# Performance work log

Hardware: AMD Instinct MI355X
Metric: run time of the kernel (lower is better)

The kernel has to match this reference:

```python
import jax, jax.numpy as jnp
import numpy as np

RADIUS = 5            # min(max(5, ceil(80/20)), 80) = 5
SPATIAL_SIGMA = 4.0
INTENSITY_SIGMA = 1.0
EPS_MEAN = 1e-5
EPS_DEN = 1e-6


def gaussian_kernel(radius, sigma, dtype):
    # norm.pdf(d/sigma)/norm.pdf(0) == exp(-d^2 / (2*sigma^2))
    x2 = jnp.arange(-radius, radius + 1, dtype=dtype) ** 2
    d2 = x2[:, None, None] + x2[None, :, None] + x2[None, None, :]
    k = jnp.exp(-d2 / (2.0 * sigma * sigma))
    return k[None, None]  # OIDHW: [1,1,2r+1,2r+1,2r+1]


def conv3d_same(x, kernel):
    # x: [B,1,H,W,D]; 'same' padding with radius on all spatial dims
    pad = [(RADIUS, RADIUS)] * 3
    return jax.lax.conv_general_dilated(
        x, kernel, window_strides=(1, 1, 1), padding=pad,
        dimension_numbers=('NCDHW', 'OIDHW', 'NCDHW'))


def setup_inputs() -> dict:
    key = jax.random.key(0)
    k1, k2 = jax.random.split(key)
    labels = jax.random.uniform(k1, (2, 4, 80, 80, 80), dtype=jnp.float32)
    inputs = jax.random.uniform(k2, (2, 1, 80, 80, 80), dtype=jnp.float32)
    return {"labels": labels, "inputs": inputs}


def reference(labels, inputs):
    N, K, H, W, D = labels.shape
    kernel = gaussian_kernel(RADIUS, SPATIAL_SIGMA, labels.dtype)

    probs = labels[:, :, None]          # [N,K,1,H,W,D]
    img = inputs[:, None]               # [N,1,C,H,W,D]

    # per-class mean intensity: [N,K,C,1,1,1]
    class_mean = (jnp.mean(img * probs, axis=(3, 4, 5), keepdims=True)
                  / (jnp.mean(probs, axis=(3, 4, 5), keepdims=True) + EPS_MEAN))
    diff = jnp.sum((img - class_mean) ** 2, axis=2)        # [N,K,H,W,D]
    weights = jnp.exp(-(diff ** 2) / (INTENSITY_SIGMA ** 2))  # [N,K,H,W,D]

    # batch the K independent single-channel 3D convs as [N*K,1,H,W,D]
    pw = (labels * weights).reshape(N * K, 1, H, W, D)
    w = weights.reshape(N * K, 1, H, W, D)
    conv_pw = conv3d_same(pw, kernel).reshape(N, K, H, W, D)
    conv_w = conv3d_same(w, kernel).reshape(N, K, H, W, D)

    numerator = jnp.sum(labels * conv_pw, axis=(2, 3, 4))   # [N,K]
    denominator = jnp.sum(labels * conv_w, axis=(2, 3, 4))  # [N,K]
    ratio = numerator / (denominator + EPS_DEN)

    # torch L1Loss(num/den, 0) = mean over batch N, summed over classes k
    loss = jnp.sum(jnp.mean(jnp.abs(ratio), axis=0))
    return K - loss
```

## Files before the change

### kernel.cpp

```cpp
#include <hip/hip_runtime.h>
#include <math.h>

#define RAD 5
#define SIDE 80
#define SLAB 6400
#define VOL 512000
#define NCH 8
#define NCLS 4
#define Q 20
#define TW 40
#define NT 2
#define C1 (SIDE*NT)
#define NBLK1 (NCH*C1)
#define TBS 22
#define NBLK2 1000
#define CPB 125

__constant__ float GW[11] = {
    0.45783336177161427f, 0.6065306597126334f, 0.7548396019890073f,
    0.8824969025845955f,  0.969233234476344f,  1.0f,
    0.969233234476344f,   0.8824969025845955f, 0.7548396019890073f,
    0.6065306597126334f,  0.45783336177161427f};

__device__ unsigned short g_bufT[(size_t)NCH * VOL];
__device__ float2 g_part1[NBLK1];
__device__ float2 g_part2[NBLK2];

__device__ __forceinline__ unsigned short f2bf(float f) {
    unsigned u = __float_as_uint(f);
    u += 0x7FFFu + ((u >> 16) & 1u);
    return (unsigned short)(u >> 16);
}
__device__ __forceinline__ float bf2f(unsigned short h) {
    return __uint_as_float((unsigned)h << 16);
}

__global__ void __launch_bounds__(256) convdw_sums_kernel(
        const float* __restrict__ labels, const float* __restrict__ img) {
    const int tile = blockIdx.x;
    const int c   = tile / C1;
    const int rem = tile % C1;
    const int h   = rem / NT;
    const int w0  = (rem % NT) * TW;
    const int n   = c >> 2;

    __shared__ float4 tB[(TW + 10) * TBS];
    __shared__ float sm[8];

    const float4* labc4 = (const float4*)(labels + ((size_t)c * SIDE + h) * SLAB);
    const float4* imgc4 = (const float4*)(img + ((size_t)n * SIDE + h) * SLAB);

    float sip = 0.f, sp = 0.f;
    for (int i = threadIdx.x; i < (TW + 10) * Q; i += 256) {
        const int r = i / Q, q = i - (i / Q) * Q;
        const int w = w0 - RAD + r;
        float a[20];
        #pragma unroll
        for (int j = 0; j < 20; ++j) a[j] = 0.f;
        if ((unsigned)w < SIDE) {
            const float4* row = labc4 + (size_t)w * Q;
            #pragma unroll
            for (int j = 0; j < 5; ++j) {
                int qq = q - 2 + j;
                if (qq >= 0 && qq < Q) {
                    float4 v = row[qq];
                    a[4 * j] = v.x; a[4 * j + 1] = v.y;
                    a[4 * j + 2] = v.z; a[4 * j + 3] = v.w;
                }
            }
            if (r >= RAD && r < RAD + TW) {
                float4 v = imgc4[(size_t)w * Q + q];
                sip += a[8] * v.x + a[9] * v.y + a[10] * v.z + a[11] * v.w;
                sp  += a[8] + a[9] + a[10] + a[11];
            }
        }
        float s0 = 0.f, s1 = 0.f, s2 = 0.f, s3 = 0.f;
        #pragma unroll
        for (int t = 0; t < 11; ++t) {
            float g = GW[t];
            s0 += g * a[t + 3]; s1 += g * a[t + 4];
            s2 += g * a[t + 5]; s3 += g * a[t + 6];
        }
        tB[r * TBS + q] = make_float4(s0, s1, s2, s3);
    }
    #pragma unroll
    for (int off = 32; off > 0; off >>= 1) {
        sip += __shfl_down(sip, off);
        sp  += __shfl_down(sp, off);
    }
    const int lane = threadIdx.x & 63;
    const int wid  = threadIdx.x >> 6;
    if (lane == 0) { sm[wid * 2] = sip; sm[wid * 2 + 1] = sp; }
    __syncthreads();
    if (threadIdx.x == 0)
        g_part1[tile] = make_float2(sm[0] + sm[2] + sm[4] + sm[6],
                                    sm[1] + sm[3] + sm[5] + sm[7]);
    ushort4* out4 = (ushort4*)g_bufT + ((size_t)c * VOL + (size_t)h * SIDE) / 4;
    for (int i = threadIdx.x; i < TW * Q; i += 256) {
        const int rl = i / Q, q = i - (i / Q) * Q;
        float sx = 0.f, sy = 0.f, sz = 0.f, sw = 0.f;
        #pragma unroll
        for (int t = 0; t < 11; ++t) {
            float g = GW[t];
            float4 v = tB[(rl + t) * TBS + q];
            sx += g * v.x; sy += g * v.y; sz += g * v.z; sw += g * v.w;
        }
        ushort4 o;
        o.x = f2bf(sx); o.y = f2bf(sy); o.z = f2bf(sz); o.w = f2bf(sw);
        out4[(size_t)(w0 + rl) * (SLAB / 4) + q] = o;
    }
}

__global__ void __launch_bounds__(256) convh_dot_kernel(
        const float* __restrict__ labels, const float* __restrict__ img) {
    const int c   = blockIdx.x / CPB;
    const int rem = (blockIdx.x % CPB) * 256 + threadIdx.x;
    const int hq  = rem / 1600;
    const int r2  = rem % 1600;
    const int w   = r2 / Q;
    const int q   = r2 % Q;
    const int h0  = hq * 4;
    const int n   = c >> 2;

    __shared__ float sm[8];
    __shared__ float s_mean;

    float a = 0.f, b = 0.f;
    for (int t = threadIdx.x; t < C1; t += 256) {
        float2 p = g_part1[c * C1 + t];
        a += p.x; b += p.y;
    }
    #pragma unroll
    for (int off = 32; off > 0; off >>= 1) {
        a += __shfl_down(a, off);
        b += __shfl_down(b, off);
    }
    const int lane = threadIdx.x & 63;
    const int wid  = threadIdx.x >> 6;
    if (lane == 0) { sm[wid * 2] = a; sm[wid * 2 + 1] = b; }
    __syncthreads();
    if (threadIdx.x == 0)
        s_mean = (sm[0] + sm[2] + sm[4] + sm[6]) /
                 (sm[1] + sm[3] + sm[5] + sm[7] + 5.12f);
    __syncthreads();
    const float mean = s_mean;

    const ushort4* bc4 = (const ushort4*)g_bufT + ((size_t)c * VOL + (size_t)w * SLAB) / 4;
    float4 win[14];
    #pragma unroll
    for (int m = 0; m < 14; ++m) {
        int hh = h0 - RAD + m;
        if ((unsigned)hh < SIDE) {
            ushort4 u = bc4[hh * Q + q];
            win[m] = make_float4(bf2f(u.x), bf2f(u.y), bf2f(u.z), bf2f(u.w));
        } else {
            win[m] = make_float4(0.f, 0.f, 0.f, 0.f);
        }
    }
    const float4* labp4 = (const float4*)labels + (size_t)c * (VOL / 4);
    const float4* imgp4 = (const float4*)img + (size_t)n * (VOL / 4);
    float num = 0.f, den = 0.f;
    #pragma unroll
    for (int k = 0; k < 4; ++k) {
        float sx = 0.f, sy = 0.f, sz = 0.f, sw = 0.f;
        #pragma unroll
        for (int t = 0; t < 11; ++t) {
            float g = GW[t];
            float4 v = win[k + t];
            sx += g * v.x; sy += g * v.y; sz += g * v.z; sw += g * v.w;
        }
        size_t gi = (size_t)(h0 + k) * (SLAB / 4) + (size_t)w * Q + q;
        float4 l = labp4[gi];
        float4 v = imgp4[gi];
        float d0 = v.x - mean, d1 = v.y - mean, d2 = v.z - mean, d3 = v.w - mean;
        float q0 = d0 * d0, q1 = d1 * d1, q2 = d2 * d2, q3 = d3 * d3;
        float e0 = __expf(-q0 * q0), e1 = __expf(-q1 * q1);
        float e2 = __expf(-q2 * q2), e3 = __expf(-q3 * q3);
        num += sx * l.x * e0 + sy * l.y * e1 + sz * l.z * e2 + sw * l.w * e3;
        den += sx * e0 + sy * e1 + sz * e2 + sw * e3;
    }
    #pragma unroll
    for (int off = 32; off > 0; off >>= 1) {
        num += __shfl_down(num, off);
        den += __shfl_down(den, off);
    }
    if (lane == 0) { sm[wid * 2] = num; sm[wid * 2 + 1] = den; }
    __syncthreads();
    if (threadIdx.x == 0)
        g_part2[blockIdx.x] = make_float2(sm[0] + sm[2] + sm[4] + sm[6],
                                          sm[1] + sm[3] + sm[5] + sm[7]);
}

__global__ void __launch_bounds__(256) final_kernel(float* __restrict__ out) {
    __shared__ float cn[NCH], cd[NCH];
    const int lane = threadIdx.x & 63;
    const int wid  = threadIdx.x >> 6;
    #pragma unroll
    for (int cc = 0; cc < 2; ++cc) {
        const int c = wid * 2 + cc;
        float a = 0.f, b = 0.f;
        for (int t = lane; t < CPB; t += 64) {
            float2 p = g_part2[c * CPB + t];
            a += p.x; b += p.y;
        }
        #pragma unroll
        for (int off = 32; off > 0; off >>= 1) {
            a += __shfl_down(a, off);
            b += __shfl_down(b, off);
        }
        if (lane == 0) { cn[c] = a; cd[c] = b; }
    }
    __syncthreads();
    if (threadIdx.x == 0) {
        float loss = 0.f;
        for (int k = 0; k < NCLS; ++k) {
            float r0 = cn[k]        / (cd[k]        + 1e-6f);
            float r1 = cn[NCLS + k] / (cd[NCLS + k] + 1e-6f);
            loss += 0.5f * (fabsf(r0) + fabsf(r1));
        }
        out[0] = (float)NCLS - loss;
    }
}

extern "C" void kernel_launch(void* const* d_in, const int* in_sizes, int n_in,
                              void* d_out, int out_size, void* d_ws, size_t ws_size,
                              hipStream_t stream) {
    const float* labels = (const float*)d_in[0];
    const float* img    = (const float*)d_in[1];
    float* out = (float*)d_out;
    (void)d_ws; (void)ws_size;

    hipLaunchKernelGGL(convdw_sums_kernel, dim3(NBLK1), dim3(256), 0, stream, labels, img);
    hipLaunchKernelGGL(convh_dot_kernel,   dim3(NBLK2), dim3(256), 0, stream, labels, img);
    hipLaunchKernelGGL(final_kernel,       dim3(1),     dim3(256), 0, stream, out);
}
```

Before: 88.42 us.

## Stage H-direction conv window in shared memory per (w, half-h) tile

After: 85.85 us. 2.9% less time.

```diff
diff --git a/kernel.cpp b/kernel.cpp
--- a/kernel.cpp
+++ b/kernel.cpp
@@ -13,8 +13,9 @@
 #define C1 (SIDE*NT)
 #define NBLK1 (NCH*C1)
 #define TBS 22
-#define NBLK2 1000
-#define CPB 125
+#define NBLK2 1280
+#define CPB 160
+#define SBS 84
 
 __constant__ float GW[11] = {
     0.45783336177161427f, 0.6065306597126334f, 0.7548396019890073f,
@@ -114,64 +115,60 @@
 __global__ void __launch_bounds__(256) convh_dot_kernel(
         const float* __restrict__ labels, const float* __restrict__ img) {
     const int c   = blockIdx.x / CPB;
-    const int rem = (blockIdx.x % CPB) * 256 + threadIdx.x;
-    const int hq  = rem / 1600;
-    const int r2  = rem % 1600;
-    const int w   = r2 / Q;
-    const int q   = r2 % Q;
-    const int h0  = hq * 4;
+    const int rw  = blockIdx.x % CPB;
+    const int w   = rw >> 1;
+    const int hh0 = (rw & 1) * 40;
     const int n   = c >> 2;
 
+    __shared__ float sB[50 * SBS];
     __shared__ float sm[8];
-    __shared__ float s_mean;
+    const int lane = threadIdx.x & 63;
+    const int wid  = threadIdx.x >> 6;
 
     float a = 0.f, b = 0.f;
-    for (int t = threadIdx.x; t < C1; t += 256) {
-        float2 p = g_part1[c * C1 + t];
-        a += p.x; b += p.y;
-    }
+    if (threadIdx.x < C1) {
+        float2 p = g_part1[c * C1 + threadIdx.x];
+        a = p.x; b = p.y;
+    }
+
+    const ushort4* src = (const ushort4*)g_bufT + ((size_t)c * VOL + (size_t)w * SLAB) / 4;
+    for (int i = threadIdx.x; i < 50 * Q; i += 256) {
+        const int row = i / Q, s = i - (i / Q) * Q;
+        const int hh = hh0 - RAD + row;
+        float4 v = make_float4(0.f, 0.f, 0.f, 0.f);
+        if ((unsigned)hh < SIDE) {
+            ushort4 u = src[hh * Q + s];
+            v = make_float4(bf2f(u.x), bf2f(u.y), bf2f(u.z), bf2f(u.w));
+        }
+        *(float4*)&sB[row * SBS + s * 4] = v;
+    }
+
     #pragma unroll
     for (int off = 32; off > 0; off >>= 1) {
         a += __shfl_down(a, off);
         b += __shfl_down(b, off);
     }
-    const int lane = threadIdx.x & 63;
-    const int wid  = threadIdx.x >> 6;
     if (lane == 0) { sm[wid * 2] = a; sm[wid * 2 + 1] = b; }
     __syncthreads();
-    if (threadIdx.x == 0)
-        s_mean = (sm[0] + sm[2] + sm[4] + sm[6]) /
-                 (sm[1] + sm[3] + sm[5] + sm[7] + 5.12f);
-    __syncthreads();
-    const float mean = s_mean;
-
-    const ushort4* bc4 = (const ushort4*)g_bufT + ((size_t)c * VOL + (size_t)w * SLAB) / 4;
-    float4 win[14];
-    #pragma unroll
-    for (int m = 0; m < 14; ++m) {
-        int hh = h0 - RAD + m;
-        if ((unsigned)hh < SIDE) {
-            ushort4 u = bc4[hh * Q + q];
-            win[m] = make_float4(bf2f(u.x), bf2f(u.y), bf2f(u.z), bf2f(u.w));
-        } else {
-            win[m] = make_float4(0.f, 0.f, 0.f, 0.f);
-        }
-    }
+    const float mean = (sm[0] + sm[2] + sm[4] + sm[6]) /
+                       (sm[1] + sm[3] + sm[5] + sm[7] + 5.12f);
+
     const float4* labp4 = (const float4*)labels + (size_t)c * (VOL / 4);
     const float4* imgp4 = (const float4*)img + (size_t)n * (VOL / 4);
     float num = 0.f, den = 0.f;
-    #pragma unroll
-    for (int k = 0; k < 4; ++k) {
+    for (int i = threadIdx.x; i < TW * Q; i += 256) {
+        const int hl = i / Q, q = i - (i / Q) * Q;
+        const int h  = hh0 + hl;
         float sx = 0.f, sy = 0.f, sz = 0.f, sw = 0.f;
         #pragma unroll
         for (int t = 0; t < 11; ++t) {
             float g = GW[t];
-            float4 v = win[k + t];
+            float4 v = *(const float4*)&sB[(hl + t) * SBS + q * 4];
             sx += g * v.x; sy += g * v.y; sz += g * v.z; sw += g * v.w;
         }
-        size_t gi = (size_t)(h0 + k) * (SLAB / 4) + (size_t)w * Q + q;
-        float4 l = labp4[gi];
-        float4 v = imgp4[gi];
+        const int li = h * (SLAB / 4) + w * Q + q;
+        float4 l = labp4[li];
+        float4 v = imgp4[li];
         float d0 = v.x - mean, d1 = v.y - mean, d2 = v.z - mean, d3 = v.w - mean;
         float q0 = d0 * d0, q1 = d1 * d1, q2 = d2 * d2, q3 = d3 * d3;
         float e0 = __expf(-q0 * q0), e1 = __expf(-q1 * q1);
@@ -184,6 +181,7 @@
         num += __shfl_down(num, off);
         den += __shfl_down(den, off);
     }
+    __syncthreads();
     if (lane == 0) { sm[wid * 2] = num; sm[wid * 2 + 1] = den; }
     __syncthreads();
     if (threadIdx.x == 0)
```
